# Kernel tuning notes

Hardware: AMD Instinct MI355X
Metric: run time of the kernel (lower is better)

## Reference

```python
import jax, jax.numpy as jnp
import numpy as np

TOP_K = 16
TAU = 1.0
LN_EPS = 1e-5
NORM_EPS = 1e-12


def setup_inputs() -> dict:
    key = jax.random.key(0)
    ks = jax.random.split(key, 8)
    B, T, V, H = 2, 1024, 32000, 1024
    inner = 2 * H
    logits = jax.random.normal(ks[0], (B, T, V), jnp.float32)
    hidden_states = jax.random.normal(ks[1], (B, T, H), jnp.float32)
    labels = jax.random.randint(ks[2], (B, T), 0, V, jnp.int32)
    future_summaries = jax.random.normal(ks[3], (B, T, H), jnp.float32)
    future_valid = jnp.ones((B, T), jnp.bool_)
    embed_weight = jax.random.normal(ks[4], (V, H), jnp.float32) * 0.02
    W1 = jax.random.normal(ks[5], (2 * H, inner), jnp.float32) * 0.02
    b1 = jnp.zeros((inner,), jnp.float32)
    W2 = jax.random.normal(ks[6], (inner, H), jnp.float32) * 0.02
    b2 = jnp.zeros((H,), jnp.float32)
    ln_g = jnp.ones((H,), jnp.float32)
    ln_b = jnp.zeros((H,), jnp.float32)
    return dict(logits=logits, hidden_states=hidden_states, labels=labels,
                future_summaries=future_summaries, future_valid=future_valid,
                embed_weight=embed_weight, W1=W1, b1=b1, W2=W2, b2=b2,
                ln_g=ln_g, ln_b=ln_b)


def _build_action_set(logits_flat, labels_flat):
    # top-k candidate ids + ground-truth id, deduped, left-packed.
    BT = logits_flat.shape[0]
    _, topk_idx = jax.lax.top_k(logits_flat, TOP_K)          # (BT, K)
    combined = jnp.concatenate([topk_idx, labels_flat[:, None]], axis=1)  # (BT, A)
    A = combined.shape[1]
    sort_order = jnp.argsort(combined, axis=1)               # stable
    sorted_idx = jnp.take_along_axis(combined, sort_order, axis=1)
    uniq_sorted = jnp.concatenate(
        [jnp.ones((BT, 1), jnp.bool_), sorted_idx[:, 1:] != sorted_idx[:, :-1]], axis=1)
    unsort = jnp.argsort(sort_order, axis=1)
    unique_mask = jnp.take_along_axis(uniq_sorted, unsort, axis=1)
    pos = jnp.cumsum(unique_mask, axis=1) - 1
    # route duplicates to a trash column A, then slice it off
    safe_pos = jnp.where(unique_mask, pos, A)
    rows = jnp.arange(BT)[:, None]
    action_indices = jnp.zeros((BT, A + 1), combined.dtype).at[rows, safe_pos].set(combined)[:, :A]
    action_mask = jnp.zeros((BT, A + 1), jnp.bool_).at[rows, safe_pos].set(True)[:, :A]
    return action_indices, action_mask


def _layernorm(x, g, b):
    mu = jnp.mean(x, axis=-1, keepdims=True)
    var = jnp.var(x, axis=-1, keepdims=True)
    return (x - mu) * jax.lax.rsqrt(var + LN_EPS) * g + b


def _normalize(x):
    n = jnp.linalg.norm(x, axis=-1, keepdims=True)
    return x / jnp.maximum(n, NORM_EPS)


def reference(logits, hidden_states, labels, future_summaries, future_valid,
              embed_weight, W1, b1, W2, b2, ln_g, ln_b):
    B, T, V = logits.shape
    H = hidden_states.shape[-1]
    logits_flat = logits.reshape(-1, V)
    hidden_flat = hidden_states.reshape(-1, H)
    labels_flat = labels.reshape(-1)
    future_flat = future_summaries.reshape(-1, H)
    valid_mask = (labels_flat != -100) & future_valid.reshape(-1)

    action_indices, action_mask = _build_action_set(
        jax.lax.stop_gradient(logits_flat), labels_flat)      # (BT, A)

    token_embeds = embed_weight[action_indices]               # (BT, A, H)
    A = token_embeds.shape[1]
    hidden_exp = jnp.broadcast_to(hidden_flat[:, None, :], token_embeds.shape)
    future_exp = jnp.broadcast_to(future_flat[:, None, :], token_embeds.shape)

    # cos_mlp head: Linear(2H, 2H) -> GELU -> Linear(2H, H) -> LayerNorm
    fused = jnp.concatenate([hidden_exp, token_embeds], axis=-1)  # (BT, A, 2H)
    h = jax.nn.gelu(jnp.einsum('baf,fi->bai', fused, W1) + b1, approximate=False)
    delta = jnp.einsum('bai,ih->bah', h, W2) + b2
    action_repr = _layernorm(delta, ln_g, ln_b)

    scores = jnp.sum(_normalize(action_repr) * _normalize(future_exp), axis=-1)  # (BT, A)
    scores = jnp.where(action_mask, scores, -1e9)
    rewards = jax.nn.softmax(scores / TAU, axis=-1) * action_mask

    act_mask_v = action_mask & valid_mask[:, None]
    log_probs = jax.nn.log_softmax(logits_flat, axis=-1)
    lp_actions = jnp.take_along_axis(log_probs, action_indices, axis=1) * act_mask_v
    loss_per_pos = -jnp.sum(jax.lax.stop_gradient(rewards) * lp_actions, axis=1)
    denom = jnp.maximum(jnp.sum(act_mask_v, axis=1), 1)
    loss_per_pos = loss_per_pos / denom * valid_mask.astype(jnp.float32)
    normalizer = jnp.maximum(jnp.sum(valid_mask.astype(jnp.float32)), 1.0)
    loss = jnp.sum(loss_per_pos) / normalizer
    return loss
```

## Files before the change

### kernel.cpp

```cpp
#include <hip/hip_runtime.h>
#include <hip/hip_bf16.h>
#include <math.h>

#define BTOT 2048
#define VV 32000
#define HH 1024
#define INNER 2048
#define NA 17
#define MTOT (BTOT * NA)
#define CAP 1088

typedef __bf16 bf16;
typedef __bf16 bf16x8 __attribute__((ext_vector_type(8)));
typedef float f32x4 __attribute__((ext_vector_type(4)));

__device__ __forceinline__ f32x4 mfma16(bf16x8 a, bf16x8 b, f32x4 c) {
    return __builtin_amdgcn_mfma_f32_16x16x32_bf16(a, b, c, 0, 0, 0);
}

__device__ __forceinline__ void gload16(const void* g, void* l) {
    __builtin_amdgcn_global_load_lds(
        (const __attribute__((address_space(1))) unsigned int*)g,
        (__attribute__((address_space(3))) unsigned int*)l, 16, 0, 0);
}

__device__ __forceinline__ bool vi_better(float va, int ia, float vb, int ib) {
    return (va > vb) || (va == vb && ia < ib);
}

__global__ __launch_bounds__(256)
void transpose_to_bf16(const float* __restrict__ src, bf16* __restrict__ dst,
                       int R, int C)
{
    __shared__ float tile[32][33];
    const int bx = blockIdx.x * 32;
    const int by = blockIdx.y * 32;
    const int tx = threadIdx.x;
    const int ty = threadIdx.y;
#pragma unroll
    for (int i = 0; i < 32; i += 8)
        tile[ty + i][tx] = src[(size_t)(by + ty + i) * C + bx + tx];
    __syncthreads();
#pragma unroll
    for (int i = 0; i < 32; i += 8)
        dst[(size_t)(bx + ty + i) * R + by + tx] = (bf16)tile[tx][ty + i];
}

__global__ __launch_bounds__(256)
void topk_lse_kernel(const float* __restrict__ logits,
                     const int* __restrict__ labels,
                     const unsigned char* __restrict__ future_valid,
                     int* __restrict__ actions,
                     int* __restrict__ amask,
                     float* __restrict__ lp,
                     int* __restrict__ rvalid,
                     int* __restrict__ validcount)
{
    const int r = blockIdx.x;
    const int t = threadIdx.x;
    const float* __restrict__ lrow = logits + (size_t)r * VV;

    __shared__ float s_cv[CAP];
    __shared__ int   s_ci[CAP];
    __shared__ float candv[256];
    __shared__ int   candi[256];
    __shared__ float s_topv[16];
    __shared__ int   s_topi[16];
    __shared__ int   s_wtid;
    __shared__ int   s_cnt;
    __shared__ float s_redv[256];
    __shared__ int   s_redi[256];
    __shared__ int   s_redp[256];

    float m1 = -INFINITY, m2 = -INFINITY;
    int   i1 = 0x7fffffff, i2 = 0x7fffffff;
    const float4* __restrict__ lrow4 = (const float4*)lrow;
    for (int i = 0; i < 32; ++i) {
        int i4 = t + 256 * i;
        if (i4 < VV / 4) {
            float4 xv = lrow4[i4];
            float xs[4] = {xv.x, xv.y, xv.z, xv.w};
#pragma unroll
            for (int cc = 0; cc < 4; ++cc) {
                float x = xs[cc];
                int idx = i4 * 4 + cc;
                bool b1 = x > m1;
                bool b2 = x > m2;
                float nm2 = b1 ? m1 : (b2 ? x : m2);
                int   ni2 = b1 ? i1 : (b2 ? idx : i2);
                m1 = b1 ? x : m1;
                i1 = b1 ? idx : i1;
                m2 = nm2; i2 = ni2;
            }
        }
    }
    candv[t] = m1; candi[t] = i1;
    if (t == 0) s_cnt = 0;
    __syncthreads();

    int cur = 0;
    for (int round = 0; round < 16; ++round) {
        if (t < 64) {
            float bv = -INFINITY; int bi = 0x7fffffff; int btid = -1;
#pragma unroll
            for (int k2 = 0; k2 < 4; ++k2) {
                int tid = t + 64 * k2;
                float v = candv[tid]; int ii = candi[tid];
                if (vi_better(v, ii, bv, bi)) { bv = v; bi = ii; btid = tid; }
            }
#pragma unroll
            for (int ms = 1; ms < 64; ms <<= 1) {
                float ov = __shfl_xor(bv, ms, 64);
                int   oi = __shfl_xor(bi, ms, 64);
                int   ot = __shfl_xor(btid, ms, 64);
                if (vi_better(ov, oi, bv, bi)) { bv = ov; bi = oi; btid = ot; }
            }
            if (t == 0) { s_topv[round] = bv; s_topi[round] = bi; s_wtid = btid; }
        }
        __syncthreads();
        if (t == s_wtid) {
            ++cur;
            candv[t] = (cur < 2) ? m2 : -INFINITY;
            candi[t] = (cur < 2) ? i2 : 0x7fffffff;
        }
        __syncthreads();
    }

    const float M  = s_topv[0];
    const float Tv = s_topv[15];
    const int   Ti = s_topi[15];

    float lsum = 0.f;
    for (int i = 0; i < 32; ++i) {
        int i4 = t + 256 * i;
        if (i4 < VV / 4) {
            float4 xv = lrow4[i4];
            float xs[4] = {xv.x, xv.y, xv.z, xv.w};
#pragma unroll
            for (int cc = 0; cc < 4; ++cc) {
                float x = xs[cc];
                int idx = i4 * 4 + cc;
                lsum += __expf(x - M);
                if (!vi_better(Tv, Ti, x, idx)) {
                    int p = atomicAdd(&s_cnt, 1);
                    if (p < CAP) { s_cv[p] = x; s_ci[p] = idx; }
                }
            }
        }
    }
    s_redv[t] = lsum;
    __syncthreads();
    for (int s = 128; s > 0; s >>= 1) {
        if (t < s) s_redv[t] += s_redv[t + s];
        __syncthreads();
    }
    const float lse = M + logf(s_redv[0]);
    int C = s_cnt; if (C > CAP) C = CAP;
    __syncthreads();

    for (int round = 0; round < 16; ++round) {
        float bv = -INFINITY; int bi = 0x7fffffff; int bp = -1;
        for (int j = t; j < C; j += 256) {
            float v = s_cv[j]; int ii = s_ci[j];
            if (vi_better(v, ii, bv, bi)) { bv = v; bi = ii; bp = j; }
        }
        s_redv[t] = bv; s_redi[t] = bi; s_redp[t] = bp;
        __syncthreads();
        if (t < 64) {
#pragma unroll
            for (int k2 = 1; k2 < 4; ++k2) {
                float v = s_redv[t + 64*k2]; int ii = s_redi[t + 64*k2];
                int pp = s_redp[t + 64*k2];
                if (vi_better(v, ii, bv, bi)) { bv = v; bi = ii; bp = pp; }
            }
#pragma unroll
            for (int ms = 1; ms < 64; ms <<= 1) {
                float ov = __shfl_xor(bv, ms, 64);
                int   oi = __shfl_xor(bi, ms, 64);
                int   op = __shfl_xor(bp, ms, 64);
                if (vi_better(ov, oi, bv, bi)) { bv = ov; bi = oi; bp = op; }
            }
            if (t == 0) {
                s_topv[round] = bv; s_topi[round] = bi;
                if (bp >= 0) { s_cv[bp] = -INFINITY; s_ci[bp] = 0x7fffffff; }
            }
        }
        __syncthreads();
    }

    int lbl = labels[r];
    if (t < 16) {
        actions[r*NA + t] = s_topi[t];
        amask[r*NA + t]   = 1;
        lp[r*NA + t]      = s_topv[t] - lse;
    } else if (t == 16) {
        bool dup = false;
#pragma unroll
        for (int k = 0; k < 16; ++k) dup = dup || (s_topi[k] == lbl);
        actions[r*NA + 16] = dup ? 0 : lbl;
        amask[r*NA + 16]   = dup ? 0 : 1;
        lp[r*NA + 16]      = dup ? 0.f : (lrow[lbl] - lse);
        bool valid = (lbl != -100) && (future_valid[r] != 0);
        rvalid[r] = valid ? 1 : 0;
        if (valid) atomicAdd(validcount, 1);
    }
}

__global__ __launch_bounds__(256)
void build_a_kernel(const float* __restrict__ hidden,
                    const float* __restrict__ embed,
                    const int* __restrict__ actions,
                    bf16* __restrict__ A, int m0)
{
    const int ml = blockIdx.x;
    const int m = m0 + ml;
    const int r = m / NA;
    const int a = m - r * NA;
    const int t = threadIdx.x;
    const float* src = (t < 128)
        ? hidden + (size_t)r * HH + t * 8
        : embed  + (size_t)actions[r*NA + a] * HH + (t - 128) * 8;
    float4 v0 = ((const float4*)src)[0];
    float4 v1 = ((const float4*)src)[1];
    bf16x8 o;
    o[0] = (bf16)v0.x; o[1] = (bf16)v0.y; o[2] = (bf16)v0.z; o[3] = (bf16)v0.w;
    o[4] = (bf16)v1.x; o[5] = (bf16)v1.y; o[6] = (bf16)v1.z; o[7] = (bf16)v1.w;
    *(bf16x8*)(A + (size_t)ml * INNER + t * 8) = o;
}

template<bool GELU>
__global__ __launch_bounds__(256, 2)
void gemm128_kernel(const bf16* __restrict__ A,
                    const bf16* __restrict__ Bt,
                    const float* __restrict__ bias,
                    bf16* __restrict__ outB,
                    float* __restrict__ outF,
                    int N)
{
    const int nb = blockIdx.x;
    const int mb = blockIdx.y;
    const int t = threadIdx.x;
    const int w = t >> 6, lane = t & 63;
    const int q = lane >> 4, c = lane & 15;
    const int wr = w >> 1, wc = w & 1;

    __shared__ __align__(16) bf16 sA[128 * 32];
    __shared__ __align__(16) bf16 sB[128 * 32];

    const int e0 = (w*2 + 0) * 512 + lane * 8;
    const int e1 = (w*2 + 1) * 512 + lane * 8;
    const bf16* gA0 = A  + (size_t)(mb*128 + (e0 >> 5)) * INNER + (e0 & 31);
    const bf16* gA1 = A  + (size_t)(mb*128 + (e1 >> 5)) * INNER + (e1 & 31);
    const bf16* gB0 = Bt + (size_t)(nb*128 + (e0 >> 5)) * INNER + (e0 & 31);
    const bf16* gB1 = Bt + (size_t)(nb*128 + (e1 >> 5)) * INNER + (e1 & 31);
    bf16* lA0 = sA + (w*2 + 0) * 512;
    bf16* lA1 = sA + (w*2 + 1) * 512;
    bf16* lB0 = sB + (w*2 + 0) * 512;
    bf16* lB1 = sB + (w*2 + 1) * 512;

    const f32x4 z4 = {0.f, 0.f, 0.f, 0.f};
    f32x4 acc[4][4];
#pragma unroll
    for (int mt = 0; mt < 4; ++mt)
#pragma unroll
        for (int nt = 0; nt < 4; ++nt) acc[mt][nt] = z4;

#pragma unroll 1
    for (int k0 = 0; k0 < INNER; k0 += 32) {
        gload16(gA0 + k0, lA0);
        gload16(gA1 + k0, lA1);
        gload16(gB0 + k0, lB0);
        gload16(gB1 + k0, lB1);
        __syncthreads();

        bf16x8 af[4], bfr[4];
#pragma unroll
        for (int mt = 0; mt < 4; ++mt)
            af[mt] = *(const bf16x8*)&sA[(wr*64 + mt*16 + c) * 32 + q*8];
#pragma unroll
        for (int nt = 0; nt < 4; ++nt)
            bfr[nt] = *(const bf16x8*)&sB[(wc*64 + nt*16 + c) * 32 + q*8];
#pragma unroll
        for (int mt = 0; mt < 4; ++mt)
#pragma unroll
            for (int nt = 0; nt < 4; ++nt)
                acc[mt][nt] = mfma16(af[mt], bfr[nt], acc[mt][nt]);
        __syncthreads();
    }

    const int mrow = mb*128 + wr*64;
    const int ncol = nb*128 + wc*64;
#pragma unroll
    for (int nt = 0; nt < 4; ++nt) {
        const int n = ncol + nt*16 + c;
        float bb = 0.f;
        if constexpr (GELU) bb = bias[n];
#pragma unroll
        for (int mt = 0; mt < 4; ++mt) {
#pragma unroll
            for (int reg = 0; reg < 4; ++reg) {
                const int m = mrow + mt*16 + q*4 + reg;
                if constexpr (GELU) {
                    const float x = acc[mt][nt][reg] + bb;
                    const float g = 0.5f * x * (1.f + erff(x * 0.70710678118654752f));
                    outB[(size_t)m * N + n] = (bf16)g;
                } else {
                    outF[(size_t)m * N + n] = acc[mt][nt][reg];
                }
            }
        }
    }
}

__global__ __launch_bounds__(256)
void ln_cos_kernel(const float* __restrict__ D,
                   const float* __restrict__ b2,
                   const float* __restrict__ ln_g,
                   const float* __restrict__ ln_b,
                   const float* __restrict__ future,
                   int m0,
                   float* __restrict__ scores)
{
    const int ml = blockIdx.x;
    const int m = m0 + ml;
    const int r = m / NA;
    const int t = threadIdx.x;
    const int w = t >> 6, lane = t & 63;
    __shared__ float s1[4], s2[4], s3[4], s4[4], s5[4];

    float4 d  = ((const float4*)(D + (size_t)ml * HH))[t];
    float4 bb = ((const float4*)b2)[t];
    d.x += bb.x; d.y += bb.y; d.z += bb.z; d.w += bb.w;

    float p1 = d.x + d.y + d.z + d.w;
    float p2 = d.x*d.x + d.y*d.y + d.z*d.z + d.w*d.w;
#pragma unroll
    for (int m2 = 1; m2 < 64; m2 <<= 1) {
        p1 += __shfl_xor(p1, m2, 64);
        p2 += __shfl_xor(p2, m2, 64);
    }
    if (lane == 0) { s1[w] = p1; s2[w] = p2; }
    __syncthreads();
    const float S1 = s1[0] + s1[1] + s1[2] + s1[3];
    const float S2 = s2[0] + s2[1] + s2[2] + s2[3];
    const float mu = S1 * (1.f / (float)HH);
    const float rstd = rsqrtf(S2 * (1.f / (float)HH) - mu*mu + 1e-5f);

    float4 g = ((const float4*)ln_g)[t];
    float4 b = ((const float4*)ln_b)[t];
    float4 f = ((const float4*)(future + (size_t)r * HH))[t];
    float4 ar;
    ar.x = (d.x - mu) * rstd * g.x + b.x;
    ar.y = (d.y - mu) * rstd * g.y + b.y;
    ar.z = (d.z - mu) * rstd * g.z + b.z;
    ar.w = (d.w - mu) * rstd * g.w + b.w;
    float paa = ar.x*ar.x + ar.y*ar.y + ar.z*ar.z + ar.w*ar.w;
    float paf = ar.x*f.x  + ar.y*f.y  + ar.z*f.z  + ar.w*f.w;
    float pff = f.x*f.x   + f.y*f.y   + f.z*f.z   + f.w*f.w;
#pragma unroll
    for (int m2 = 1; m2 < 64; m2 <<= 1) {
        paa += __shfl_xor(paa, m2, 64);
        paf += __shfl_xor(paf, m2, 64);
        pff += __shfl_xor(pff, m2, 64);
    }
    if (lane == 0) { s3[w] = paa; s4[w] = paf; s5[w] = pff; }
    __syncthreads();
    if (t == 0) {
        const float Saa = s3[0] + s3[1] + s3[2] + s3[3];
        const float Saf = s4[0] + s4[1] + s4[2] + s4[3];
        const float Sff = s5[0] + s5[1] + s5[2] + s5[3];
        const float anorm = fmaxf(sqrtf(Saa), 1e-12f);
        const float fnorm = fmaxf(sqrtf(Sff), 1e-12f);
        scores[m] = Saf / (anorm * fnorm);
    }
}

__global__ __launch_bounds__(256)
void loss_kernel(const float* __restrict__ scores,
                 const int* __restrict__ amask,
                 const float* __restrict__ lp,
                 const int* __restrict__ rvalid,
                 const int* __restrict__ validcount,
                 float* __restrict__ out)
{
    const int r = blockIdx.x * blockDim.x + threadIdx.x;
    if (r >= BTOT) return;
    float sc[NA];
    float mx = -INFINITY;
#pragma unroll
    for (int a = 0; a < NA; ++a) {
        sc[a] = amask[r*NA + a] ? scores[r*NA + a] : -1e9f;
        mx = fmaxf(mx, sc[a]);
    }
    float ex[NA]; float ses = 0.f;
#pragma unroll
    for (int a = 0; a < NA; ++a) { ex[a] = __expf(sc[a] - mx); ses += ex[a]; }
    const int validr = rvalid[r];
    float acc = 0.f; int denom = 0;
#pragma unroll
    for (int a = 0; a < NA; ++a) {
        const int mk = amask[r*NA + a];
        const int mv = (mk && validr) ? 1 : 0;
        const float rw = (ex[a] / ses) * (float)mk;
        acc += rw * lp[r*NA + a] * (float)mv;
        denom += mv;
    }
    const float lossr = -acc / (float)(denom > 0 ? denom : 1) * (float)validr;
    atomicAdd(out, lossr / fmaxf((float)(*validcount), 1.f));
}

extern "C" void kernel_launch(void* const* d_in, const int* in_sizes, int n_in,
                              void* d_out, int out_size, void* d_ws, size_t ws_size,
                              hipStream_t stream)
{
    const float* logits        = (const float*)d_in[0];
    const float* hidden        = (const float*)d_in[1];
    const int*   labels        = (const int*)d_in[2];
    const float* future        = (const float*)d_in[3];
    const unsigned char* fvld  = (const unsigned char*)d_in[4];
    const float* embed         = (const float*)d_in[5];
    const float* W1f           = (const float*)d_in[6];
    const float* b1            = (const float*)d_in[7];
    const float* W2f           = (const float*)d_in[8];
    const float* b2            = (const float*)d_in[9];
    const float* ln_g          = (const float*)d_in[10];
    const float* ln_b          = (const float*)d_in[11];
    float* out = (float*)d_out;

    char* ws = (char*)d_ws;
    size_t off = 0;
    bf16* W1T = (bf16*)(ws + off); off += (size_t)INNER * INNER * 2;
    bf16* W2T = (bf16*)(ws + off); off += (size_t)HH * INNER * 2;
    int*   validcount = (int*)(ws + off);   off += 256;
    int*   actions    = (int*)(ws + off);   off += (size_t)MTOT * 4;
    int*   amask      = (int*)(ws + off);   off += (size_t)MTOT * 4;
    float* lp         = (float*)(ws + off); off += (size_t)MTOT * 4;
    int*   rvalid     = (int*)(ws + off);   off += (size_t)BTOT * 4;
    float* scores     = (float*)(ws + off); off += (size_t)MTOT * 4;
    off = (off + 255) & ~(size_t)255;

    size_t rem = (ws_size > off) ? (ws_size - off) : 0;
    long long cap_blocks = (long long)(rem / ((size_t)8192 * 128));
    int slab_blocks = (cap_blocks > (MTOT/128)) ? (MTOT/128) : (int)cap_blocks;
    if (slab_blocks < 1) slab_blocks = 1;
    const int slab_rows_max = slab_blocks * 128;

    bf16*  Abuf = (bf16*)(ws + off);
    float* Dbuf = (float*)Abuf;
    bf16*  Ybuf = (bf16*)(ws + off + (size_t)slab_rows_max * 4096);

    (void)hipMemsetAsync(d_out, 0, sizeof(float), stream);
    (void)hipMemsetAsync(validcount, 0, 16, stream);

    transpose_to_bf16<<<dim3(INNER/32, INNER/32), dim3(32, 8), 0, stream>>>(W1f, W1T, INNER, INNER);
    transpose_to_bf16<<<dim3(HH/32,    INNER/32), dim3(32, 8), 0, stream>>>(W2f, W2T, INNER, HH);

    topk_lse_kernel<<<BTOT, 256, 0, stream>>>(logits, labels, fvld,
                                              actions, amask, lp, rvalid, validcount);

    for (int m0 = 0; m0 < MTOT; m0 += slab_rows_max) {
        const int rows = (MTOT - m0 < slab_rows_max) ? (MTOT - m0) : slab_rows_max;
        const int nbm = rows / 128;
        build_a_kernel<<<rows, 256, 0, stream>>>(hidden, embed, actions, Abuf, m0);
        gemm128_kernel<true ><<<dim3(INNER/128, nbm), 256, 0, stream>>>(
            Abuf, W1T, b1, Ybuf, nullptr, INNER);
        gemm128_kernel<false><<<dim3(HH/128, nbm), 256, 0, stream>>>(
            Ybuf, W2T, nullptr, nullptr, Dbuf, HH);
        ln_cos_kernel<<<rows, 256, 0, stream>>>(Dbuf, b2, ln_g, ln_b, future, m0, scores);
    }

    loss_kernel<<<(BTOT + 255) / 256, 256, 0, stream>>>(scores, amask, lp,
                                                        rvalid, validcount, out);
}
```

Measured before the change: 1.204 ms.

## Hoist hidden-state half of first MLP GEMM out of per-action loop

```diff
diff --git a/kernel.cpp b/kernel.cpp
--- a/kernel.cpp
+++ b/kernel.cpp
@@ -44,6 +44,18 @@
 #pragma unroll
     for (int i = 0; i < 32; i += 8)
         dst[(size_t)(bx + ty + i) * R + by + tx] = (bf16)tile[tx][ty + i];
+}
+
+__global__ __launch_bounds__(256)
+void cast_hidden_kernel(const float* __restrict__ hidden, bf16* __restrict__ hb)
+{
+    const size_t i = ((size_t)blockIdx.x * 256 + threadIdx.x) * 8;
+    float4 v0 = ((const float4*)(hidden + i))[0];
+    float4 v1 = ((const float4*)(hidden + i))[1];
+    bf16x8 o;
+    o[0] = (bf16)v0.x; o[1] = (bf16)v0.y; o[2] = (bf16)v0.z; o[3] = (bf16)v0.w;
+    o[4] = (bf16)v1.x; o[5] = (bf16)v1.y; o[6] = (bf16)v1.z; o[7] = (bf16)v1.w;
+    *(bf16x8*)(hb + i) = o;
 }
 
 __global__ __launch_bounds__(256)
@@ -207,38 +219,40 @@
 }
 
 __global__ __launch_bounds__(256)
-void build_a_kernel(const float* __restrict__ hidden,
-                    const float* __restrict__ embed,
-                    const int* __restrict__ actions,
-                    bf16* __restrict__ A, int m0)
-{
-    const int ml = blockIdx.x;
-    const int m = m0 + ml;
-    const int r = m / NA;
-    const int a = m - r * NA;
+void build_embed_kernel(const float* __restrict__ embed,
+                        const int* __restrict__ actions,
+                        bf16* __restrict__ AE, int m0)
+{
     const int t = threadIdx.x;
-    const float* src = (t < 128)
-        ? hidden + (size_t)r * HH + t * 8
-        : embed  + (size_t)actions[r*NA + a] * HH + (t - 128) * 8;
+    const int ml = blockIdx.x * 2 + (t >> 7);
+    const int gm = m0 + ml;
+    const int r = gm / NA;
+    const int a = gm - r * NA;
+    const int tt = t & 127;
+    const float* src = embed + (size_t)actions[r*NA + a] * HH + tt * 8;
     float4 v0 = ((const float4*)src)[0];
     float4 v1 = ((const float4*)src)[1];
     bf16x8 o;
     o[0] = (bf16)v0.x; o[1] = (bf16)v0.y; o[2] = (bf16)v0.z; o[3] = (bf16)v0.w;
     o[4] = (bf16)v1.x; o[5] = (bf16)v1.y; o[6] = (bf16)v1.z; o[7] = (bf16)v1.w;
-    *(bf16x8*)(A + (size_t)ml * INNER + t * 8) = o;
-}
-
-template<bool GELU>
+    *(bf16x8*)(AE + (size_t)ml * HH + tt * 8) = o;
+}
+
+template<int MODE>
 __global__ __launch_bounds__(256, 2)
-void gemm128_kernel(const bf16* __restrict__ A,
-                    const bf16* __restrict__ Bt,
-                    const float* __restrict__ bias,
-                    bf16* __restrict__ outB,
-                    float* __restrict__ outF,
-                    int N)
-{
-    const int nb = blockIdx.x;
-    const int mb = blockIdx.y;
+void gemm128(const bf16* __restrict__ A, int lda,
+             const bf16* __restrict__ Bt, int ldb, int koff, int K,
+             const float* __restrict__ extra,
+             bf16* __restrict__ outB, float* __restrict__ outF,
+             int ldo, int nbx, int m0)
+{
+    const int nwg = gridDim.x;
+    const int per = nwg >> 3;
+    const int id  = blockIdx.x;
+    const int sid = (id & 7) * per + (id >> 3);
+    const int nb = sid % nbx;
+    const int mb = sid / nbx;
+
     const int t = threadIdx.x;
     const int w = t >> 6, lane = t & 63;
     const int q = lane >> 4, c = lane & 15;
@@ -249,10 +263,10 @@
 
     const int e0 = (w*2 + 0) * 512 + lane * 8;
     const int e1 = (w*2 + 1) * 512 + lane * 8;
-    const bf16* gA0 = A  + (size_t)(mb*128 + (e0 >> 5)) * INNER + (e0 & 31);
-    const bf16* gA1 = A  + (size_t)(mb*128 + (e1 >> 5)) * INNER + (e1 & 31);
-    const bf16* gB0 = Bt + (size_t)(nb*128 + (e0 >> 5)) * INNER + (e0 & 31);
-    const bf16* gB1 = Bt + (size_t)(nb*128 + (e1 >> 5)) * INNER + (e1 & 31);
+    const bf16* gA0 = A  + (size_t)(mb*128 + (e0 >> 5)) * lda + (e0 & 31);
+    const bf16* gA1 = A  + (size_t)(mb*128 + (e1 >> 5)) * lda + (e1 & 31);
+    const bf16* gB0 = Bt + (size_t)(nb*128 + (e0 >> 5)) * ldb + koff + (e0 & 31);
+    const bf16* gB1 = Bt + (size_t)(nb*128 + (e1 >> 5)) * ldb + koff + (e1 & 31);
     bf16* lA0 = sA + (w*2 + 0) * 512;
     bf16* lA1 = sA + (w*2 + 1) * 512;
     bf16* lB0 = sB + (w*2 + 0) * 512;
@@ -266,7 +280,7 @@
         for (int nt = 0; nt < 4; ++nt) acc[mt][nt] = z4;
 
 #pragma unroll 1
-    for (int k0 = 0; k0 < INNER; k0 += 32) {
+    for (int k0 = 0; k0 < K; k0 += 32) {
         gload16(gA0 + k0, lA0);
         gload16(gA1 + k0, lA1);
         gload16(gB0 + k0, lB0);
@@ -294,18 +308,22 @@
     for (int nt = 0; nt < 4; ++nt) {
         const int n = ncol + nt*16 + c;
         float bb = 0.f;
-        if constexpr (GELU) bb = bias[n];
+        if constexpr (MODE == 2) bb = extra[n];
 #pragma unroll
         for (int mt = 0; mt < 4; ++mt) {
 #pragma unroll
             for (int reg = 0; reg < 4; ++reg) {
                 const int m = mrow + mt*16 + q*4 + reg;
-                if constexpr (GELU) {
-                    const float x = acc[mt][nt][reg] + bb;
+                float x = acc[mt][nt][reg];
+                if constexpr (MODE == 0) {
+                    outF[(size_t)m * ldo + n] = x;
+                } else if constexpr (MODE == 1) {
+                    const int gr = (m0 + m) / NA;
+                    x += extra[(size_t)gr * INNER + n];
                     const float g = 0.5f * x * (1.f + erff(x * 0.70710678118654752f));
-                    outB[(size_t)m * N + n] = (bf16)g;
+                    outB[(size_t)m * ldo + n] = (bf16)g;
                 } else {
-                    outF[(size_t)m * N + n] = acc[mt][nt][reg];
+                    outF[(size_t)m * ldo + n] = x + bb;
                 }
             }
         }
@@ -429,8 +447,10 @@
 
     char* ws = (char*)d_ws;
     size_t off = 0;
-    bf16* W1T = (bf16*)(ws + off); off += (size_t)INNER * INNER * 2;
-    bf16* W2T = (bf16*)(ws + off); off += (size_t)HH * INNER * 2;
+    bf16*  W1T   = (bf16*)(ws + off);  off += (size_t)INNER * INNER * 2;
+    bf16*  W2T   = (bf16*)(ws + off);  off += (size_t)HH * INNER * 2;
+    bf16*  hidB  = (bf16*)(ws + off);  off += (size_t)BTOT * HH * 2;
+    float* Hpre  = (float*)(ws + off); off += (size_t)BTOT * INNER * 4;
     int*   validcount = (int*)(ws + off);   off += 256;
     int*   actions    = (int*)(ws + off);   off += (size_t)MTOT * 4;
     int*   amask      = (int*)(ws + off);   off += (size_t)MTOT * 4;
@@ -440,20 +460,24 @@
     off = (off + 255) & ~(size_t)255;
 
     size_t rem = (ws_size > off) ? (ws_size - off) : 0;
-    long long cap_blocks = (long long)(rem / ((size_t)8192 * 128));
+    long long cap_blocks = (long long)(rem / ((size_t)10240 * 128));
     int slab_blocks = (cap_blocks > (MTOT/128)) ? (MTOT/128) : (int)cap_blocks;
     if (slab_blocks < 1) slab_blocks = 1;
     const int slab_rows_max = slab_blocks * 128;
 
-    bf16*  Abuf = (bf16*)(ws + off);
-    float* Dbuf = (float*)Abuf;
-    bf16*  Ybuf = (bf16*)(ws + off + (size_t)slab_rows_max * 4096);
+    bf16*  AEbuf = (bf16*)(ws + off);
+    bf16*  Ybuf  = (bf16*)(ws + off + (size_t)slab_rows_max * 2048);
+    float* Dbuf  = (float*)(ws + off + (size_t)slab_rows_max * (2048 + 4096));
 
     (void)hipMemsetAsync(d_out, 0, sizeof(float), stream);
     (void)hipMemsetAsync(validcount, 0, 16, stream);
 
     transpose_to_bf16<<<dim3(INNER/32, INNER/32), dim3(32, 8), 0, stream>>>(W1f, W1T, INNER, INNER);
     transpose_to_bf16<<<dim3(HH/32,    INNER/32), dim3(32, 8), 0, stream>>>(W2f, W2T, INNER, HH);
+    cast_hidden_kernel<<<(BTOT*HH)/2048, 256, 0, stream>>>(hidden, hidB);
+
+    gemm128<2><<<(INNER/128) * (BTOT/128), 256, 0, stream>>>(
+        hidB, HH, W1T, INNER, 0, HH, b1, nullptr, Hpre, INNER, INNER/128, 0);
 
     topk_lse_kernel<<<BTOT, 256, 0, stream>>>(logits, labels, fvld,
                                               actions, amask, lp, rvalid, validcount);
@@ -461,11 +485,11 @@
     for (int m0 = 0; m0 < MTOT; m0 += slab_rows_max) {
         const int rows = (MTOT - m0 < slab_rows_max) ? (MTOT - m0) : slab_rows_max;
         const int nbm = rows / 128;
-        build_a_kernel<<<rows, 256, 0, stream>>>(hidden, embed, actions, Abuf, m0);
-        gemm128_kernel<true ><<<dim3(INNER/128, nbm), 256, 0, stream>>>(
-            Abuf, W1T, b1, Ybuf, nullptr, INNER);
-        gemm128_kernel<false><<<dim3(HH/128, nbm), 256, 0, stream>>>(
-            Ybuf, W2T, nullptr, nullptr, Dbuf, HH);
+        build_embed_kernel<<<rows/2, 256, 0, stream>>>(embed, actions, AEbuf, m0);
+        gemm128<1><<<(INNER/128) * nbm, 256, 0, stream>>>(
+            AEbuf, HH, W1T, INNER, HH, HH, Hpre, Ybuf, nullptr, INNER, INNER/128, m0);
+        gemm128<0><<<(HH/128) * nbm, 256, 0, stream>>>(
+            Ybuf, INNER, W2T, INNER, 0, INNER, nullptr, nullptr, Dbuf, HH, HH/128, 0);
         ln_cos_kernel<<<rows, 256, 0, stream>>>(Dbuf, b2, ln_g, ln_b, future, m0, scores);
     }
 
```

New measurement: 1.111 ms. 1.08x faster.
